# Kernel tuning notes

Hardware: AMD Instinct MI355X
Metric: run time of the kernel (lower is better)

Reference implementation:

```python
import jax, jax.numpy as jnp
import numpy as np


def _batch_pairwise_dist(x, y):
    # x: [B, Nx, D] (gts), y: [B, Ny, D] (preds) -> P: [B, Nx, Ny] squared L2
    rx = jnp.sum(x * x, axis=-1)  # [B, Nx]
    ry = jnp.sum(y * y, axis=-1)  # [B, Ny]
    zz = jnp.einsum('bnd,bmd->bnm', x, y)  # [B, Nx, Ny]
    return rx[:, :, None] + ry[:, None, :] - 2.0 * zz


def setup_inputs() -> dict:
    key = jax.random.key(0)
    k1, k2, k3 = jax.random.split(key, 3)
    B, Ngt, Npred, D = 4, 4096, 4096, 3
    preds = jax.random.normal(k1, (B, Npred, D), dtype=jnp.float32)
    gts = jax.random.normal(k2, (B, Ngt, D), dtype=jnp.float32)
    mask = jax.random.randint(k3, (B, Ngt), 0, 2).astype(jnp.bool_)
    return {"preds": preds, "gts": gts, "mask": mask}


def reference(preds, gts, mask):
    # P[b, i, j] = ||gts[b,i] - preds[b,j]||^2
    P = _batch_pairwise_dist(gts, preds)  # [B, Ngt, Npred]
    # Directional term 1: for each pred point, min over VALID gt points.
    P_masked = jnp.where(mask[:, :, None], P, jnp.inf)  # invalid gt rows -> +inf
    loss_1 = jnp.sum(jnp.min(P_masked, axis=1))
    # Directional term 2: for each VALID gt point, min over all pred points.
    mins_gt = jnp.min(P, axis=2)  # [B, Ngt]
    loss_2 = jnp.sum(jnp.where(mask, mins_gt, 0.0))
    return loss_1 + loss_2
```

## Files before the change

### kernel.cpp

```cpp
#include <hip/hip_runtime.h>

#define NBATCH 4
#define NPTS   4096
#define XPT    8
#define XCHUNK (256 * XPT)
#define NXC    (NPTS / XCHUNK)
#define YCHUNK 128
#define NPAIR  (YCHUNK / 2)
#define NYC    (NPTS / YCHUNK)
#define BIGF   1e30f

typedef float v2f __attribute__((ext_vector_type(2)));

__global__ __launch_bounds__(256)
void chamfer_min_kernel(const float* __restrict__ preds,
                        const float* __restrict__ gts,
                        const int* __restrict__ mask,
                        float* __restrict__ partial,
                        float* __restrict__ out) {
    const int zc  = blockIdx.z;
    const int dir = zc >> 2;
    const int b   = zc & 3;
    const int tid = threadIdx.x;

    if ((zc | blockIdx.x | blockIdx.y | tid) == 0) out[0] = 0.0f;

    const float* X = (dir == 0 ? preds : gts) + (size_t)b * NPTS * 3;
    const float* Y = (dir == 0 ? gts : preds) + (size_t)b * NPTS * 3;

    __shared__ float4 sp[2 * NPAIR];
    const int cbase = blockIdx.y * YCHUNK;
    if (tid < NPAIR) {
        const int ja = cbase + 2 * tid;
        const int jb = ja + 1;
        const float xa = Y[ja * 3 + 0], ya = Y[ja * 3 + 1], za = Y[ja * 3 + 2];
        const float xb = Y[jb * 3 + 0], yb = Y[jb * 3 + 1], zb = Y[jb * 3 + 2];
        float ra = xa * xa + ya * ya + za * za;
        float rb = xb * xb + yb * yb + zb * zb;
        if (dir == 0) {
            if (mask[b * NPTS + ja] == 0) ra = BIGF;
            if (mask[b * NPTS + jb] == 0) rb = BIGF;
        }
        sp[2 * tid + 0] = make_float4(xa, xb, ya, yb);
        sp[2 * tid + 1] = make_float4(za, zb, ra, rb);
    }

    v2f A0[XPT], A1[XPT], A2[XPT];
    float rx[XPT], m[XPT];
    const int xbase = blockIdx.x * XCHUNK + tid;
    #pragma unroll
    for (int i = 0; i < XPT; ++i) {
        const int x = xbase + i * 256;
        const float v0 = X[x * 3 + 0], v1 = X[x * 3 + 1], v2 = X[x * 3 + 2];
        rx[i] = v0 * v0 + v1 * v1 + v2 * v2;
        const float s0 = -2.0f * v0, s1 = -2.0f * v1, s2 = -2.0f * v2;
        A0[i] = (v2f){s0, s0}; A1[i] = (v2f){s1, s1}; A2[i] = (v2f){s2, s2};
        m[i] = BIGF;
    }
    __syncthreads();

    #pragma unroll 2
    for (int j = 0; j < NPAIR; ++j) {
        const float4 E0 = sp[2 * j + 0];
        const float4 E1 = sp[2 * j + 1];
        const v2f X2 = (v2f){E0.x, E0.y};
        const v2f Y2 = (v2f){E0.z, E0.w};
        const v2f Z2 = (v2f){E1.x, E1.y};
        const v2f R2 = (v2f){E1.z, E1.w};
        #pragma unroll
        for (int i = 0; i < XPT; ++i) {
            v2f t = __builtin_elementwise_fma(A2[i], Z2, R2);
            t = __builtin_elementwise_fma(A1[i], Y2, t);
            t = __builtin_elementwise_fma(A0[i], X2, t);
            m[i] = fminf(fminf(m[i], t.x), t.y);
        }
    }

    float* prow = partial + ((size_t)zc * NYC + blockIdx.y) * NPTS + xbase;
    #pragma unroll
    for (int i = 0; i < XPT; ++i)
        prow[i * 256] = rx[i] + m[i];
}

__global__ __launch_bounds__(256)
void chamfer_reduce_kernel(const float* __restrict__ partial,
                           const int* __restrict__ mask,
                           float* __restrict__ out) {
    const int gid = blockIdx.x * blockDim.x + threadIdx.x;
    const int p4  = gid * 4;
    const int dir = p4 >> 14;
    const int b   = (p4 >> 12) & 3;
    const int x   = p4 & 4095;
    const int zc  = dir * NBATCH + b;

    const float4* base = (const float4*)(partial + (size_t)zc * NYC * NPTS + x);
    float4 m4 = base[0];
    #pragma unroll
    for (int r = 1; r < NYC; ++r) {
        const float4 v = base[(size_t)r * (NPTS / 4)];
        m4.x = fminf(m4.x, v.x); m4.y = fminf(m4.y, v.y);
        m4.z = fminf(m4.z, v.z); m4.w = fminf(m4.w, v.w);
    }

    float acc;
    if (dir == 1) {
        const int4 mk = *(const int4*)(mask + b * NPTS + x);
        acc = (mk.x ? m4.x : 0.0f) + (mk.y ? m4.y : 0.0f)
            + (mk.z ? m4.z : 0.0f) + (mk.w ? m4.w : 0.0f);
    } else {
        acc = m4.x + m4.y + m4.z + m4.w;
    }

    #pragma unroll
    for (int off = 32; off > 0; off >>= 1)
        acc += __shfl_down(acc, off, 64);

    __shared__ float wsum[4];
    if ((threadIdx.x & 63) == 0) wsum[threadIdx.x >> 6] = acc;
    __syncthreads();
    if (threadIdx.x == 0)
        atomicAdd(out, wsum[0] + wsum[1] + wsum[2] + wsum[3]);
}

extern "C" void kernel_launch(void* const* d_in, const int* in_sizes, int n_in,
                              void* d_out, int out_size, void* d_ws, size_t ws_size,
                              hipStream_t stream) {
    const float* preds = (const float*)d_in[0];
    const float* gts   = (const float*)d_in[1];
    const int*   mask  = (const int*)d_in[2];
    float* out = (float*)d_out;

    float* partial = (float*)d_ws;

    dim3 grid(NXC, NYC, 2 * NBATCH);
    chamfer_min_kernel<<<grid, 256, 0, stream>>>(preds, gts, mask, partial, out);

    chamfer_reduce_kernel<<<(2 * NBATCH * NPTS / 4) / 256, 256, 0, stream>>>(
        partial, mask, out);
}
```

Baseline: 21.31 us.

## Fuse min and reduction kernels with flag-based inter-block completion

Replaces the two-kernel pipeline with one kernel. The first Y-chunk block of each column waits on per-block flags for the other chunks' partial minima, reduces them, and publishes a column sum. A single final block spin-waits on column flags and writes the total. Tile shapes also change (fewer X points per thread, larger Y chunk) while keeping the same block count. The aim is to drop the second launch and its dependency gap. In exchange it relies on all blocks being co-resident and on the flag workspace starting zeroed.

Measured after the change: 26.87 us. +26.1%, slower.

```diff
diff --git a/kernel.cpp b/kernel.cpp
--- a/kernel.cpp
+++ b/kernel.cpp
@@ -2,34 +2,43 @@
 
 #define NBATCH 4
 #define NPTS   4096
-#define XPT    8
+#define XPT    4
 #define XCHUNK (256 * XPT)
 #define NXC    (NPTS / XCHUNK)
-#define YCHUNK 128
+#define YCHUNK 256
 #define NPAIR  (YCHUNK / 2)
 #define NYC    (NPTS / YCHUNK)
+#define NBLK   (8 * NYC * NXC)
+#define NCOL   (8 * NXC)
 #define BIGF   1e30f
 
 typedef float v2f __attribute__((ext_vector_type(2)));
 
+#define LOAD_AG(p)    __hip_atomic_load((p),  __ATOMIC_RELAXED, __HIP_MEMORY_SCOPE_AGENT)
+#define STORE_AG(p,v) __hip_atomic_store((p),(v), __ATOMIC_RELAXED, __HIP_MEMORY_SCOPE_AGENT)
+
 __global__ __launch_bounds__(256)
-void chamfer_min_kernel(const float* __restrict__ preds,
-                        const float* __restrict__ gts,
-                        const int* __restrict__ mask,
-                        float* __restrict__ partial,
-                        float* __restrict__ out) {
-    const int zc  = blockIdx.z;
+void chamfer_fused_kernel(const float* __restrict__ preds,
+                          const float* __restrict__ gts,
+                          const int* __restrict__ mask,
+                          float* __restrict__ partial,
+                          float* __restrict__ colsum,
+                          unsigned* __restrict__ flag1,
+                          unsigned* __restrict__ flag2,
+                          float* __restrict__ out) {
+    const int bid = blockIdx.x;
+    const int tid = threadIdx.x;
+    const int xc  = bid & (NXC - 1);
+    const int yc  = (bid >> 2) & (NYC - 1);
+    const int zc  = bid >> 6;
     const int dir = zc >> 2;
     const int b   = zc & 3;
-    const int tid = threadIdx.x;
-
-    if ((zc | blockIdx.x | blockIdx.y | tid) == 0) out[0] = 0.0f;
 
     const float* X = (dir == 0 ? preds : gts) + (size_t)b * NPTS * 3;
     const float* Y = (dir == 0 ? gts : preds) + (size_t)b * NPTS * 3;
 
     __shared__ float4 sp[2 * NPAIR];
-    const int cbase = blockIdx.y * YCHUNK;
+    const int cbase = yc * YCHUNK;
     if (tid < NPAIR) {
         const int ja = cbase + 2 * tid;
         const int jb = ja + 1;
@@ -47,7 +56,7 @@
 
     v2f A0[XPT], A1[XPT], A2[XPT];
     float rx[XPT], m[XPT];
-    const int xbase = blockIdx.x * XCHUNK + tid;
+    const int xbase = xc * XCHUNK + tid;
     #pragma unroll
     for (int i = 0; i < XPT; ++i) {
         const int x = xbase + i * 256;
@@ -76,50 +85,88 @@
         }
     }
 
-    float* prow = partial + ((size_t)zc * NYC + blockIdx.y) * NPTS + xbase;
-    #pragma unroll
-    for (int i = 0; i < XPT; ++i)
-        prow[i * 256] = rx[i] + m[i];
-}
+    {
+        float* prow = partial + ((size_t)zc * NYC + yc) * NPTS + xbase;
+        #pragma unroll
+        for (int i = 0; i < XPT; ++i)
+            STORE_AG(prow + i * 256, rx[i] + m[i]);
+    }
+    __syncthreads();
 
-__global__ __launch_bounds__(256)
-void chamfer_reduce_kernel(const float* __restrict__ partial,
-                           const int* __restrict__ mask,
-                           float* __restrict__ out) {
-    const int gid = blockIdx.x * blockDim.x + threadIdx.x;
-    const int p4  = gid * 4;
-    const int dir = p4 >> 14;
-    const int b   = (p4 >> 12) & 3;
-    const int x   = p4 & 4095;
-    const int zc  = dir * NBATCH + b;
+    if (yc != 0) {
+        if (tid == 0)
+            __hip_atomic_store(&flag1[bid], 1u, __ATOMIC_RELEASE,
+                               __HIP_MEMORY_SCOPE_AGENT);
+        return;
+    }
 
-    const float4* base = (const float4*)(partial + (size_t)zc * NYC * NPTS + x);
-    float4 m4 = base[0];
+    if (tid < NYC - 1) {
+        while (LOAD_AG(&flag1[bid + NXC * (tid + 1)]) != 1u)
+            __builtin_amdgcn_s_sleep(4);
+    }
+    __syncthreads();
+    __threadfence();
+
+    const float4* colbase =
+        (const float4*)(partial + (size_t)zc * NYC * NPTS + xc * XCHUNK) + tid;
+    float4 m4 = colbase[0];
     #pragma unroll
     for (int r = 1; r < NYC; ++r) {
-        const float4 v = base[(size_t)r * (NPTS / 4)];
+        const float4 v = colbase[(size_t)r * (NPTS / 4)];
         m4.x = fminf(m4.x, v.x); m4.y = fminf(m4.y, v.y);
         m4.z = fminf(m4.z, v.z); m4.w = fminf(m4.w, v.w);
     }
 
     float acc;
+    const int x0 = xc * XCHUNK + 4 * tid;
     if (dir == 1) {
-        const int4 mk = *(const int4*)(mask + b * NPTS + x);
+        const int4 mk = *(const int4*)(mask + b * NPTS + x0);
         acc = (mk.x ? m4.x : 0.0f) + (mk.y ? m4.y : 0.0f)
             + (mk.z ? m4.z : 0.0f) + (mk.w ? m4.w : 0.0f);
     } else {
         acc = m4.x + m4.y + m4.z + m4.w;
     }
-
     #pragma unroll
     for (int off = 32; off > 0; off >>= 1)
         acc += __shfl_down(acc, off, 64);
 
     __shared__ float wsum[4];
-    if ((threadIdx.x & 63) == 0) wsum[threadIdx.x >> 6] = acc;
+    __shared__ float s_total;
+    if ((tid & 63) == 0) wsum[tid >> 6] = acc;
     __syncthreads();
-    if (threadIdx.x == 0)
-        atomicAdd(out, wsum[0] + wsum[1] + wsum[2] + wsum[3]);
+    if (tid == 0) s_total = wsum[0] + wsum[1] + wsum[2] + wsum[3];
+    __syncthreads();
+
+    const int col = zc * NXC + xc;
+    if (col != 0) {
+        if (tid == 0) {
+            STORE_AG(&colsum[col], s_total);
+            __hip_atomic_store(&flag2[col], 1u, __ATOMIC_RELEASE,
+                               __HIP_MEMORY_SCOPE_AGENT);
+        }
+        if (tid < NYC - 1)
+            STORE_AG(&flag1[bid + NXC * (tid + 1)], 0u);
+        return;
+    }
+
+    if (tid >= 1 && tid < NCOL) {
+        while (LOAD_AG(&flag2[tid]) != 1u)
+            __builtin_amdgcn_s_sleep(4);
+    }
+    __syncthreads();
+    __threadfence();
+
+    float v = 0.0f;
+    if (tid >= 1 && tid < NCOL) v = LOAD_AG(&colsum[tid]);
+    if (tid == 0) v = s_total;
+    #pragma unroll
+    for (int off = 16; off > 0; off >>= 1)
+        v += __shfl_down(v, off, 32);
+    if (tid == 0) out[0] = v;
+
+    if (tid >= 1 && tid < NCOL) STORE_AG(&flag2[tid], 0u);
+    if (tid < NYC - 1)
+        STORE_AG(&flag1[bid + NXC * (tid + 1)], 0u);
 }
 
 extern "C" void kernel_launch(void* const* d_in, const int* in_sizes, int n_in,
@@ -130,11 +177,11 @@
     const int*   mask  = (const int*)d_in[2];
     float* out = (float*)d_out;
 
-    float* partial = (float*)d_ws;
+    float*    partial = (float*)d_ws;
+    float*    colsum  = partial + (size_t)8 * NYC * NPTS;
+    unsigned* flag1   = (unsigned*)(colsum + NCOL);
+    unsigned* flag2   = flag1 + NBLK;
 
-    dim3 grid(NXC, NYC, 2 * NBATCH);
-    chamfer_min_kernel<<<grid, 256, 0, stream>>>(preds, gts, mask, partial, out);
-
-    chamfer_reduce_kernel<<<(2 * NBATCH * NPTS / 4) / 256, 256, 0, stream>>>(
-        partial, mask, out);
+    chamfer_fused_kernel<<<NBLK, 256, 0, stream>>>(
+        preds, gts, mask, partial, colsum, flag1, flag2, out);
 }
```
